# Optimization experiments

Measured on AMD Instinct MI355X. Metric: run time of the kernel, lower is better.

The kernel has to match this reference:

```python
import jax, jax.numpy as jnp
import numpy as np

RMS_EPS = 1.1920928955078125e-07  # torch.finfo(float32).eps, nn.RMSNorm default when eps=None


def setup_inputs() -> dict:
    key = jax.random.key(0)
    ks = jax.random.split(key, 7)
    B, T, C, Wh, E, K = 8, 4096, 256, 1024, 8, 2
    return {
        "x": jax.random.normal(ks[0], (B, T, C), dtype=jnp.float32),
        "rms_weight": jnp.ones((C,), dtype=jnp.float32),
        "W1": jax.random.normal(ks[1], (E, C, Wh), dtype=jnp.float32),
        "b1": jax.random.normal(ks[2], (E, Wh), dtype=jnp.float32),
        "W2": jax.random.normal(ks[3], (E, Wh, C), dtype=jnp.float32),
        "b2": jax.random.normal(ks[4], (E, C), dtype=jnp.float32),
        "expert_ids": jax.random.randint(ks[5], (B, T, K), 0, E, dtype=jnp.int64),
    }


def reference(x, rms_weight, W1, b1, W2, b2, expert_ids):
    # RMSNorm over last dim (torch nn.RMSNorm, eps = float32 eps)
    xn = x * jax.lax.rsqrt(jnp.mean(x * x, axis=-1, keepdims=True) + RMS_EPS) * rms_weight
    # Per-expert 2-layer MLP. The torch code gathers per-token weight copies then bmm's;
    # mathematically identical (and far cheaper in memory) is: run every expert densely,
    # then gather the K selected expert outputs per token.
    h = jax.nn.gelu(jnp.einsum("btc,ecw->btew", xn, W1) + b1, approximate=False)  # [B,T,E,Wh]
    y = jnp.einsum("btew,ewc->btec", h, W2) + b2  # [B,T,E,C]
    # gather selected experts: [B,T,K,C]; dropout p is 0.0 (eval) -> identity
    out = jnp.take_along_axis(y, expert_ids[..., None], axis=2)
    return out
```

## Files before the change

### kernel.cpp

```cpp
#include <hip/hip_runtime.h>
#include <cstdint>

typedef unsigned short ushort_t;
typedef __bf16 bf16x8 __attribute__((ext_vector_type(8)));
typedef ushort_t u16x8 __attribute__((ext_vector_type(8)));
typedef float f32x4 __attribute__((ext_vector_type(4)));
typedef uint32_t u32x4 __attribute__((ext_vector_type(4)));

#define RMS_EPS 1.1920928955078125e-07f

__device__ __forceinline__ ushort_t f2bf(float f) {
  uint32_t u = __builtin_bit_cast(uint32_t, f);
  u += 0x7fffu + ((u >> 16) & 1u);
  return (ushort_t)(u >> 16);
}

__device__ __forceinline__ void g2l16(const ushort_t* g, ushort_t* l) {
  __builtin_amdgcn_global_load_lds(
      (const __attribute__((address_space(1))) uint32_t*)g,
      (__attribute__((address_space(3))) uint32_t*)l, 16, 0, 0);
}

__device__ __forceinline__ f32x4 mfma32(bf16x8 a, bf16x8 b, f32x4 c) {
  return __builtin_amdgcn_mfma_f32_16x16x32_bf16(a, b, c, 0, 0, 0);
}

__device__ __forceinline__ float gelu1(float v) {
  float vc = fminf(fmaxf(v, -2.9f), 2.9f);
  float x2 = vc * vc;
  float p = fmaf(-0.000414256f, x2, 0.0107517f);
  p = fmaf(p, x2, -0.1136149f);
  p = fmaf(p, x2, 0.786301f);
  float E = vc * p;
  float t = 0.5f * v;
  return fmaf(t, E, t);
}

__global__ __launch_bounds__(256) void fused_pre(
    const float* __restrict__ x, const float* __restrict__ rw,
    ushort_t* __restrict__ xn,
    const float* __restrict__ W1, const float* __restrict__ W2,
    ushort_t* __restrict__ w1f, ushort_t* __restrict__ w2f,
    const int* __restrict__ eids, int* __restrict__ cnt,
    int* __restrict__ lists) {
  __shared__ ushort_t tile[64][130];
  __shared__ int lcnt[8], lbase[8];
  int bid = blockIdx.x;
  int t = threadIdx.x;

  if (bid < 8192) {
    int token = bid * 4 + (t >> 6);
    int lane = t & 63;
    const float4* row = reinterpret_cast<const float4*>(x + (size_t)token * 256);
    float4 v = row[lane];
    float s = v.x * v.x + v.y * v.y + v.z * v.z + v.w * v.w;
#pragma unroll
    for (int off = 1; off < 64; off <<= 1) s += __shfl_xor(s, off);
    float inv = rsqrtf(s * (1.0f / 256.0f) + RMS_EPS);
    const float4* wr = reinterpret_cast<const float4*>(rw);
    float4 wv = wr[lane];
    ushort4 o;
    o.x = f2bf(v.x * inv * wv.x);
    o.y = f2bf(v.y * inv * wv.y);
    o.z = f2bf(v.z * inv * wv.z);
    o.w = f2bf(v.w * inv * wv.w);
    *reinterpret_cast<ushort4*>(xn + (size_t)token * 256 + lane * 4) = o;
  } else if (bid < 8704) {
    int b = bid - 8192;
    int isW2 = b >= 256;
    const float* src; ushort_t* dst; int e, kt, wt, rs;
    if (!isW2) { e = b >> 5; kt = (b >> 3) & 3; wt = b & 7; src = W1; dst = w1f; rs = 1024; }
    else { b -= 256; e = b >> 5; kt = (b >> 1) & 15; wt = b & 1; src = W2; dst = w2f; rs = 256; }
    int k0 = kt * 64, c0 = wt * 128;
    const float* sb = src + ((size_t)e << 18) + (size_t)k0 * rs + c0;
#pragma unroll
    for (int i = 0; i < 8; ++i) {
      int f = i * 1024 + t * 4;
      int r = f >> 7, c = f & 127;
      float4 v = *reinterpret_cast<const float4*>(sb + (size_t)r * rs + c);
      ushort2 lo, hi;
      lo.x = f2bf(v.x); lo.y = f2bf(v.y); hi.x = f2bf(v.z); hi.y = f2bf(v.w);
      *reinterpret_cast<ushort2*>(&tile[r][c]) = lo;
      *reinterpret_cast<ushort2*>(&tile[r][c + 2]) = hi;
    }
    __syncthreads();
    int lane = t & 63, l16 = lane & 15, quad = lane >> 4;
    int wave = t >> 6;
    if (!isW2) {
#pragma unroll
      for (int p = 0; p < 4; ++p) {
        int u = p * 256 + t;
        int kk2 = (u >> 9) & 1;
        int rr = kk2 * 32 + quad * 8;
        int nt = (u >> 6) & 1, chL = (u >> 7) & 3;
        int cc = chL * 32 + nt * 16 + l16;
        u16x8 o;
#pragma unroll
        for (int j = 0; j < 8; ++j) o[j] = tile[rr + j][cc];
        size_t U = ((size_t)e * 32768) + (size_t)(wt * 4 + chL) * 1024 + (kt * 2 + kk2) * 128 + nt * 64 + lane;
        *reinterpret_cast<u16x8*>(dst + U * 8) = o;
      }
    } else {
#pragma unroll
      for (int p = 0; p < 4; ++p) {
        int u = p * 4 + wave;
        int chL = u >> 3, ctL = u & 7;
        int cc = ctL * 16 + l16;
        u16x8 o;
#pragma unroll
        for (int j = 0; j < 4; ++j) o[j] = tile[chL * 32 + quad * 4 + j][cc];
#pragma unroll
        for (int j = 0; j < 4; ++j) o[4 + j] = tile[chL * 32 + 16 + quad * 4 + j][cc];
        size_t U = (((size_t)(e * 32 + kt * 2 + chL) * 16) + (wt * 8 + ctL)) * 64 + lane;
        *reinterpret_cast<u16x8*>(dst + U * 8) = o;
      }
    }
  } else {
    if (t < 8) lcnt[t] = 0;
    __syncthreads();
    int p = (bid - 8704) * 256 + t;
    int e = eids[p];
    int lpos = atomicAdd(&lcnt[e], 1);
    __syncthreads();
    if (t < 8) lbase[t] = atomicAdd(&cnt[t], lcnt[t]);
    __syncthreads();
    lists[e * 65536 + lbase[e] + lpos] = p;
  }
}

__global__ __launch_bounds__(256, 3) void moe_mlp(
    const ushort_t* __restrict__ xn,
    const ushort_t* __restrict__ w1f,
    const ushort_t* __restrict__ w2f,
    const float* __restrict__ b1,
    const float* __restrict__ b2,
    const int* __restrict__ cnt,
    const int* __restrict__ lists,
    float* __restrict__ out)
{
  __shared__ __align__(16) ushort_t w1b[2][8192];
  __shared__ __align__(16) ushort_t w2b[8192];

  int cpx = gridDim.x >> 3;
  int flat = (blockIdx.x & 7) * cpx + (blockIdx.x >> 3);

  int e = -1, tile = 0, accum = 0, n_e = 0;
#pragma unroll
  for (int i = 0; i < 8; ++i) {
    int c = cnt[i];
    int ti = (c + 63) >> 6;
    if (e < 0 && flat < accum + ti) { e = i; tile = flat - accum; n_e = c; }
    accum += ti;
  }
  if (e < 0) return;
  int start = tile * 64;

  int tid = threadIdx.x;
  int wave = tid >> 6, lane = tid & 63, l16 = lane & 15, quad = lane >> 4;

  const ushort_t* w1e = w1f + ((size_t)e << 18);
  const ushort_t* w2e = w2f + ((size_t)e << 18);
  const int* le = lists + e * 65536;

  int gi = start + wave * 16 + l16;
  int pr = le[(gi < n_e) ? gi : 0];

#pragma unroll
  for (int j = 0; j < 4; ++j) {
    int p = j * 4 + wave;
    g2l16(w1e + p * 512 + lane * 8, &w1b[0][p * 512]);
  }

  bf16x8 afr[8];
  {
    const u32x4* ar = reinterpret_cast<const u32x4*>(xn + (size_t)(pr >> 1) * 256);
#pragma unroll
    for (int kk = 0; kk < 8; ++kk)
      afr[kk] = __builtin_bit_cast(bf16x8, ar[kk * 4 + quad]);
  }

  f32x4 acc[16];
#pragma unroll
  for (int ct = 0; ct < 16; ++ct) acc[ct] = (f32x4){0.f, 0.f, 0.f, 0.f};

  const float* b1e = b1 + e * 1024;

  for (int ch = 0; ch < 32; ++ch) {
    int cur = ch & 1;
    asm volatile("s_waitcnt vmcnt(0)" ::: "memory");
    __builtin_amdgcn_s_barrier();
    __builtin_amdgcn_sched_barrier(0);

    int w0 = ch * 32;
    f32x4 bia0 = *reinterpret_cast<const f32x4*>(b1e + w0 + quad * 4);
    f32x4 bia1 = *reinterpret_cast<const f32x4*>(b1e + w0 + 16 + quad * 4);
    __builtin_amdgcn_sched_barrier(0);

    {
      const ushort_t* n2 = w2e + ch * 8192;
#pragma unroll
      for (int j = 0; j < 4; ++j) {
        int p = j * 4 + wave;
        g2l16(n2 + p * 512 + lane * 8, &w2b[p * 512]);
      }
    }
    __builtin_amdgcn_sched_barrier(0);
    if (ch + 1 < 32) {
      const ushort_t* n1 = w1e + (ch + 1) * 8192;
#pragma unroll
      for (int j = 0; j < 4; ++j) {
        int p = j * 4 + wave;
        g2l16(n1 + p * 512 + lane * 8, &w1b[cur ^ 1][p * 512]);
      }
    }
    __builtin_amdgcn_sched_barrier(0);

    const ushort_t* l1 = w1b[cur];
    f32x4 ht0 = (f32x4){0.f, 0.f, 0.f, 0.f};
    f32x4 ht1 = (f32x4){0.f, 0.f, 0.f, 0.f};
    __builtin_amdgcn_s_setprio(1);
#pragma unroll
    for (int kk = 0; kk < 8; ++kk) {
      bf16x8 wA = *reinterpret_cast<const bf16x8*>(l1 + ((kk * 2 + 0) * 64 + lane) * 8);
      bf16x8 wB = *reinterpret_cast<const bf16x8*>(l1 + ((kk * 2 + 1) * 64 + lane) * 8);
      ht0 = mfma32(wA, afr[kk], ht0);
      ht1 = mfma32(wB, afr[kk], ht1);
    }
    __builtin_amdgcn_s_setprio(0);

    u16x8 hp;
#pragma unroll
    for (int rr = 0; rr < 4; ++rr) {
      hp[rr]     = f2bf(gelu1(ht0[rr] + bia0[rr]));
      hp[4 + rr] = f2bf(gelu1(ht1[rr] + bia1[rr]));
    }
    bf16x8 hF = __builtin_bit_cast(bf16x8, hp);

    if (ch < 31) {
      asm volatile("s_waitcnt vmcnt(4)" ::: "memory");
    } else {
      asm volatile("s_waitcnt vmcnt(0)" ::: "memory");
    }
    __builtin_amdgcn_s_barrier();
    __builtin_amdgcn_sched_barrier(0);

    __builtin_amdgcn_s_setprio(1);
#pragma unroll
    for (int ct = 0; ct < 16; ++ct) {
      bf16x8 wq = *reinterpret_cast<const bf16x8*>(w2b + (ct * 64 + lane) * 8);
      acc[ct] = mfma32(wq, hF, acc[ct]);
    }
    __builtin_amdgcn_s_setprio(0);
  }

  const float* b2e = b2 + e * 256;
  if (gi < n_e) {
    float* orow = out + (size_t)pr * 256;
#pragma unroll
    for (int ct = 0; ct < 16; ++ct) {
      f32x4 bv = *reinterpret_cast<const f32x4*>(b2e + ct * 16 + quad * 4);
      f32x4 o = acc[ct] + bv;
      *reinterpret_cast<f32x4*>(orow + ct * 16 + quad * 4) = o;
    }
  }
}

extern "C" void kernel_launch(void* const* d_in, const int* in_sizes, int n_in,
                              void* d_out, int out_size, void* d_ws, size_t ws_size,
                              hipStream_t stream) {
  const float* x  = (const float*)d_in[0];
  const float* rw = (const float*)d_in[1];
  const float* W1 = (const float*)d_in[2];
  const float* b1 = (const float*)d_in[3];
  const float* W2 = (const float*)d_in[4];
  const float* b2 = (const float*)d_in[5];
  const int* eids = (const int*)d_in[6];
  float* out = (float*)d_out;

  char* ws = (char*)d_ws;
  ushort_t* xn  = (ushort_t*)(ws);
  ushort_t* w1f = (ushort_t*)(ws + 16777216);
  ushort_t* w2f = (ushort_t*)(ws + 20971520);
  int* cnt      = (int*)(ws + 25165824);
  int* lists    = (int*)(ws + 25166080);

  hipMemsetAsync(cnt, 0, 8 * sizeof(int), stream);
  fused_pre<<<8960, 256, 0, stream>>>(x, rw, xn, W1, W2, w1f, w2f, eids, cnt, lists);
  moe_mlp<<<1032, 256, 0, stream>>>(xn, w1f, w2f, b1, b2, cnt, lists, out);
}
```

Baseline: 219.5 us.

## Fuse RMSNorm into MoE kernel and read W2 fragments directly from global

Moves the RMSNorm of each token into the MoE MLP kernel: it loads fp32 x rows, reduces within the wave, and builds the bf16 A fragments in registers. This removes the separate normalization blocks and the bf16 xn round trip through global memory. It also drops LDS staging of W2, so each wave reads W2 fragments straight from global (L2) memory, and it simplifies synchronisation to a plain __syncthreads while removing setprio and sched barriers. The cost is redundant norm work, since each token row is normalized once per selected expert. The second GEMM's loads are also no longer overlapped or shared through LDS.

```diff
diff --git a/kernel.cpp b/kernel.cpp
--- a/kernel.cpp
+++ b/kernel.cpp
@@ -37,8 +37,6 @@
 }
 
 __global__ __launch_bounds__(256) void fused_pre(
-    const float* __restrict__ x, const float* __restrict__ rw,
-    ushort_t* __restrict__ xn,
     const float* __restrict__ W1, const float* __restrict__ W2,
     ushort_t* __restrict__ w1f, ushort_t* __restrict__ w2f,
     const int* __restrict__ eids, int* __restrict__ cnt,
@@ -48,25 +46,8 @@
   int bid = blockIdx.x;
   int t = threadIdx.x;
 
-  if (bid < 8192) {
-    int token = bid * 4 + (t >> 6);
-    int lane = t & 63;
-    const float4* row = reinterpret_cast<const float4*>(x + (size_t)token * 256);
-    float4 v = row[lane];
-    float s = v.x * v.x + v.y * v.y + v.z * v.z + v.w * v.w;
-#pragma unroll
-    for (int off = 1; off < 64; off <<= 1) s += __shfl_xor(s, off);
-    float inv = rsqrtf(s * (1.0f / 256.0f) + RMS_EPS);
-    const float4* wr = reinterpret_cast<const float4*>(rw);
-    float4 wv = wr[lane];
-    ushort4 o;
-    o.x = f2bf(v.x * inv * wv.x);
-    o.y = f2bf(v.y * inv * wv.y);
-    o.z = f2bf(v.z * inv * wv.z);
-    o.w = f2bf(v.w * inv * wv.w);
-    *reinterpret_cast<ushort4*>(xn + (size_t)token * 256 + lane * 4) = o;
-  } else if (bid < 8704) {
-    int b = bid - 8192;
+  if (bid < 512) {
+    int b = bid;
     int isW2 = b >= 256;
     const float* src; ushort_t* dst; int e, kt, wt, rs;
     if (!isW2) { e = b >> 5; kt = (b >> 3) & 3; wt = b & 7; src = W1; dst = w1f; rs = 1024; }
@@ -118,7 +99,7 @@
   } else {
     if (t < 8) lcnt[t] = 0;
     __syncthreads();
-    int p = (bid - 8704) * 256 + t;
+    int p = (bid - 512) * 256 + t;
     int e = eids[p];
     int lpos = atomicAdd(&lcnt[e], 1);
     __syncthreads();
@@ -129,7 +110,8 @@
 }
 
 __global__ __launch_bounds__(256, 3) void moe_mlp(
-    const ushort_t* __restrict__ xn,
+    const float* __restrict__ x,
+    const float* __restrict__ rw,
     const ushort_t* __restrict__ w1f,
     const ushort_t* __restrict__ w2f,
     const float* __restrict__ b1,
@@ -139,7 +121,6 @@
     float* __restrict__ out)
 {
   __shared__ __align__(16) ushort_t w1b[2][8192];
-  __shared__ __align__(16) ushort_t w2b[8192];
 
   int cpx = gridDim.x >> 3;
   int flat = (blockIdx.x & 7) * cpx + (blockIdx.x >> 3);
@@ -173,10 +154,30 @@
 
   bf16x8 afr[8];
   {
-    const u32x4* ar = reinterpret_cast<const u32x4*>(xn + (size_t)(pr >> 1) * 256);
-#pragma unroll
-    for (int kk = 0; kk < 8; ++kk)
-      afr[kk] = __builtin_bit_cast(bf16x8, ar[kk * 4 + quad]);
+    const float* xr = x + (size_t)(pr >> 1) * 256 + quad * 8;
+    float4 ra[8], rb[8];
+    float s = 0.f;
+#pragma unroll
+    for (int kk = 0; kk < 8; ++kk) {
+      ra[kk] = *reinterpret_cast<const float4*>(xr + kk * 32);
+      rb[kk] = *reinterpret_cast<const float4*>(xr + kk * 32 + 4);
+      s += ra[kk].x * ra[kk].x + ra[kk].y * ra[kk].y + ra[kk].z * ra[kk].z + ra[kk].w * ra[kk].w;
+      s += rb[kk].x * rb[kk].x + rb[kk].y * rb[kk].y + rb[kk].z * rb[kk].z + rb[kk].w * rb[kk].w;
+    }
+    s += __shfl_xor(s, 16);
+    s += __shfl_xor(s, 32);
+    float inv = rsqrtf(s * (1.0f / 256.0f) + RMS_EPS);
+#pragma unroll
+    for (int kk = 0; kk < 8; ++kk) {
+      float4 wa = *reinterpret_cast<const float4*>(rw + kk * 32 + quad * 8);
+      float4 wb = *reinterpret_cast<const float4*>(rw + kk * 32 + quad * 8 + 4);
+      u16x8 t0;
+      t0[0] = f2bf(ra[kk].x * inv * wa.x); t0[1] = f2bf(ra[kk].y * inv * wa.y);
+      t0[2] = f2bf(ra[kk].z * inv * wa.z); t0[3] = f2bf(ra[kk].w * inv * wa.w);
+      t0[4] = f2bf(rb[kk].x * inv * wb.x); t0[5] = f2bf(rb[kk].y * inv * wb.y);
+      t0[6] = f2bf(rb[kk].z * inv * wb.z); t0[7] = f2bf(rb[kk].w * inv * wb.w);
+      afr[kk] = __builtin_bit_cast(bf16x8, t0);
+    }
   }
 
   f32x4 acc[16];
@@ -187,24 +188,8 @@
 
   for (int ch = 0; ch < 32; ++ch) {
     int cur = ch & 1;
-    asm volatile("s_waitcnt vmcnt(0)" ::: "memory");
-    __builtin_amdgcn_s_barrier();
-    __builtin_amdgcn_sched_barrier(0);
-
-    int w0 = ch * 32;
-    f32x4 bia0 = *reinterpret_cast<const f32x4*>(b1e + w0 + quad * 4);
-    f32x4 bia1 = *reinterpret_cast<const f32x4*>(b1e + w0 + 16 + quad * 4);
-    __builtin_amdgcn_sched_barrier(0);
-
-    {
-      const ushort_t* n2 = w2e + ch * 8192;
-#pragma unroll
-      for (int j = 0; j < 4; ++j) {
-        int p = j * 4 + wave;
-        g2l16(n2 + p * 512 + lane * 8, &w2b[p * 512]);
-      }
-    }
-    __builtin_amdgcn_sched_barrier(0);
+    __syncthreads();
+
     if (ch + 1 < 32) {
       const ushort_t* n1 = w1e + (ch + 1) * 8192;
 #pragma unroll
@@ -213,12 +198,10 @@
         g2l16(n1 + p * 512 + lane * 8, &w1b[cur ^ 1][p * 512]);
       }
     }
-    __builtin_amdgcn_sched_barrier(0);
 
     const ushort_t* l1 = w1b[cur];
     f32x4 ht0 = (f32x4){0.f, 0.f, 0.f, 0.f};
     f32x4 ht1 = (f32x4){0.f, 0.f, 0.f, 0.f};
-    __builtin_amdgcn_s_setprio(1);
 #pragma unroll
     for (int kk = 0; kk < 8; ++kk) {
       bf16x8 wA = *reinterpret_cast<const bf16x8*>(l1 + ((kk * 2 + 0) * 64 + lane) * 8);
@@ -226,7 +209,10 @@
       ht0 = mfma32(wA, afr[kk], ht0);
       ht1 = mfma32(wB, afr[kk], ht1);
     }
-    __builtin_amdgcn_s_setprio(0);
+
+    int w0 = ch * 32;
+    f32x4 bia0 = *reinterpret_cast<const f32x4*>(b1e + w0 + quad * 4);
+    f32x4 bia1 = *reinterpret_cast<const f32x4*>(b1e + w0 + 16 + quad * 4);
 
     u16x8 hp;
 #pragma unroll
@@ -236,21 +222,12 @@
     }
     bf16x8 hF = __builtin_bit_cast(bf16x8, hp);
 
-    if (ch < 31) {
-      asm volatile("s_waitcnt vmcnt(4)" ::: "memory");
-    } else {
-      asm volatile("s_waitcnt vmcnt(0)" ::: "memory");
-    }
-    __builtin_amdgcn_s_barrier();
-    __builtin_amdgcn_sched_barrier(0);
-
-    __builtin_amdgcn_s_setprio(1);
+    const ushort_t* w2g = w2e + ch * 8192;
 #pragma unroll
     for (int ct = 0; ct < 16; ++ct) {
-      bf16x8 wq = *reinterpret_cast<const bf16x8*>(w2b + (ct * 64 + lane) * 8);
+      bf16x8 wq = *reinterpret_cast<const bf16x8*>(w2g + (ct * 64 + lane) * 8);
       acc[ct] = mfma32(wq, hF, acc[ct]);
     }
-    __builtin_amdgcn_s_setprio(0);
   }
 
   const float* b2e = b2 + e * 256;
@@ -278,13 +255,12 @@
   float* out = (float*)d_out;
 
   char* ws = (char*)d_ws;
-  ushort_t* xn  = (ushort_t*)(ws);
-  ushort_t* w1f = (ushort_t*)(ws + 16777216);
-  ushort_t* w2f = (ushort_t*)(ws + 20971520);
-  int* cnt      = (int*)(ws + 25165824);
-  int* lists    = (int*)(ws + 25166080);
+  ushort_t* w1f = (ushort_t*)(ws);
+  ushort_t* w2f = (ushort_t*)(ws + 4194304);
+  int* cnt      = (int*)(ws + 8388608);
+  int* lists    = (int*)(ws + 8388864);
 
   hipMemsetAsync(cnt, 0, 8 * sizeof(int), stream);
-  fused_pre<<<8960, 256, 0, stream>>>(x, rw, xn, W1, W2, w1f, w2f, eids, cnt, lists);
-  moe_mlp<<<1032, 256, 0, stream>>>(xn, w1f, w2f, b1, b2, cnt, lists, out);
-}
+  fused_pre<<<768, 256, 0, stream>>>(W1, W2, w1f, w2f, eids, cnt, lists);
+  moe_mlp<<<1032, 256, 0, stream>>>(x, rw, w1f, w2f, b1, b2, cnt, lists, out);
+}
```

Result: slower. 272.0 us (+23.9%).
